# Optimization experiments

Measured on AMD Instinct MI355X. Metric: run time of the kernel, lower is better.

## Reference

```python
import jax, jax.numpy as jnp
import numpy as np

N = 100000
E = 3200000
IN_DIM = 128
OUT_DIM = 128
BN_EPS = 1e-5
LEAKY_SLOPE = 0.01


def setup_inputs() -> dict:
    key = jax.random.key(0)
    ks = jax.random.split(key, 6)
    fea = jax.random.normal(ks[0], (N, IN_DIM), dtype=jnp.float32)
    edges = jax.random.randint(ks[1], (2, E), 0, N, dtype=jnp.int64)
    Wlin = jax.random.normal(ks[2], (IN_DIM, IN_DIM), dtype=jnp.float32) * (1.0 / np.sqrt(IN_DIM))
    blin = jax.random.normal(ks[3], (IN_DIM,), dtype=jnp.float32) * 0.01
    gamma = jnp.ones((IN_DIM,), dtype=jnp.float32)
    beta = jnp.zeros((IN_DIM,), dtype=jnp.float32)
    Wg = jax.random.normal(ks[4], (OUT_DIM, IN_DIM), dtype=jnp.float32) * (1.0 / np.sqrt(IN_DIM))
    bg = jnp.zeros((OUT_DIM,), dtype=jnp.float32)
    return {"fea": fea, "edges": edges, "Wlin": Wlin, "blin": blin,
            "gamma": gamma, "beta": beta, "Wg": Wg, "bg": bg}


def reference(fea, edges, Wlin, blin, gamma, beta, Wg, bg):
    n = fea.shape[0]
    # Linear (in_dim -> in_dim)
    x = fea @ Wlin.T + blin
    # BatchNorm1d, training-mode batch statistics over the node dimension
    mean = jnp.mean(x, axis=0)
    var = jnp.var(x, axis=0)
    x = gamma * (x - mean) * jax.lax.rsqrt(var + BN_EPS) + beta
    # Dropout(p=0.0) is identity; LeakyReLU
    x = jnp.where(x >= 0, x, LEAKY_SLOPE * x)
    # GCNConv: h = x W^T, then D^-1/2 (A+I) D^-1/2 aggregation + bias
    h = x @ Wg.T  # [N, out_dim]
    self_idx = jnp.arange(n, dtype=edges.dtype)
    src = jnp.concatenate([edges[0], self_idx])
    dst = jnp.concatenate([edges[1], self_idx])
    deg = jax.ops.segment_sum(jnp.ones_like(dst, dtype=h.dtype), dst, num_segments=n)
    dinv = jnp.where(deg > 0, jax.lax.rsqrt(deg), 0.0)
    norm = dinv[src] * dinv[dst]  # [E+N]
    msgs = norm[:, None] * h[src]  # [E+N, out_dim]
    out = jax.ops.segment_sum(msgs, dst, num_segments=n) + bg
    # LogSoftmax over feature dim
    return jax.nn.log_softmax(out, axis=1)
```

## Files before the change

kernel.cpp:

```cpp
#include <hip/hip_runtime.h>
#include <math.h>

#define LEAKY 0.01f
#define BN_EPS 1e-5f
#define NBLK 480
#define EBUF 10240

typedef unsigned int uint;
typedef float f32x2 __attribute__((ext_vector_type(2)));
typedef float f32x4 __attribute__((ext_vector_type(4)));
typedef short bf16x8 __attribute__((ext_vector_type(8)));

__device__ __forceinline__ float bflo(uint v) { return __uint_as_float(v << 16); }
__device__ __forceinline__ float bfhi(uint v) { return __uint_as_float(v & 0xffff0000u); }
__device__ __forceinline__ uint packbf(float a, float b) {
    uint ua = __float_as_uint(a), ub = __float_as_uint(b);
    ua += 0x7fffu + ((ua >> 16) & 1u);
    ub += 0x7fffu + ((ub >> 16) & 1u);
    return (ua >> 16) | (ub & 0xffff0000u);
}

__device__ __forceinline__ int detect_i64(const int* __restrict__ raw) {
    int t = threadIdx.x & 63;
    unsigned long long b = __ballot(raw[2 * t + 1] != 0);
    return b == 0ull;
}

__device__ __forceinline__ void build_bbase_wide(const int* __restrict__ btot,
                                                 int NBUK, int* bb, int* sd)
{
    const int t = threadIdx.x;
    int a0 = 0, a1 = 0, s = 0;
    if (t < 256) {
        a0 = (2 * t     < NBUK) ? btot[2 * t]     : 0;
        a1 = (2 * t + 1 < NBUK) ? btot[2 * t + 1] : 0;
        s = a0 + a1;
        sd[t] = s;
    }
    __syncthreads();
    for (int o = 1; o < 256; o <<= 1) {
        int u = (t >= o && t < 256) ? sd[t - o] : 0;
        __syncthreads();
        if (t < 256) sd[t] += u;
        __syncthreads();
    }
    if (t < 256) {
        int ex = sd[t] - s;
        bb[2 * t]     = ex;
        bb[2 * t + 1] = ex + a0;
    }
    __syncthreads();
}

__global__ __launch_bounds__(256) void k_prep(const float* __restrict__ Wlin,
                                              const float* __restrict__ Wg,
                                              uint* __restrict__ Wlinb,
                                              uint* __restrict__ Wgb,
                                              float* __restrict__ sumsr)
{
    const int idx = blockIdx.x * 256 + threadIdx.x;
    if (blockIdx.x < 32) sumsr[blockIdx.x * 256 + threadIdx.x] = 0.f;
    if (idx < 8192) {
        Wlinb[idx] = packbf(Wlin[2 * idx], Wlin[2 * idx + 1]);
    } else {
        int j = idx - 8192;
        Wgb[j] = packbf(Wg[2 * j], Wg[2 * j + 1]);
    }
}

__global__ __launch_bounds__(256) void k_front(const float* __restrict__ fea,
                                               const uint* __restrict__ Wb,
                                               const float* __restrict__ bias,
                                               uint* __restrict__ xb,
                                               float* __restrict__ sumsr,
                                               const void* __restrict__ edges, int E,
                                               int* __restrict__ histm,
                                               int NBUK, int N, int G_lin)
{
    __shared__ uint smem[4352];
    const int tid = threadIdx.x;

    if ((int)blockIdx.x >= G_lin) {
        const int bid = blockIdx.x - G_lin;
        int* hh = (int*)smem;
        for (int b = tid; b < 512; b += 256) hh[b] = 0;
        const int isI64 = detect_i64((const int*)edges);
        __syncthreads();
        const long long* e64 = (const long long*)edges;
        const int*       e32 = (const int*)edges;
        const int chunk = (E + NBLK - 1) / NBLK;
        const int lo = bid * chunk;
        const int hi = min(lo + chunk, E);
        for (int e = lo + tid; e < hi; e += 256) {
            int dst = isI64 ? (int)e64[(size_t)E + e] : e32[(size_t)E + e];
            atomicAdd(&hh[dst >> 8], 1);
        }
        __syncthreads();
        for (int b = tid; b < NBUK; b += 256)
            histm[(size_t)b * NBLK + bid] = hh[b];
        return;
    }

    const int r0   = blockIdx.x * 64;
    const int lane = tid & 63;
    const int w    = tid >> 6;
    const int fr   = lane & 15;
    const int fk   = lane >> 4;
    const int gr_a = r0 + w * 16 + fr;

    bf16x8 a[4];
    #pragma unroll
    for (int kk = 0; kk < 4; ++kk) {
        float4 q0 = make_float4(0.f, 0.f, 0.f, 0.f), q1 = q0;
        if (gr_a < N) {
            const float* fp = &fea[(size_t)gr_a * 128 + 32 * kk + 8 * fk];
            q0 = *reinterpret_cast<const float4*>(fp);
            q1 = *reinterpret_cast<const float4*>(fp + 4);
        }
        uint4 uu = make_uint4(packbf(q0.x, q0.y), packbf(q0.z, q0.w),
                              packbf(q1.x, q1.y), packbf(q1.z, q1.w));
        a[kk] = *reinterpret_cast<bf16x8*>(&uu);
    }

    f32x4 acc[8] = {};
    #pragma unroll
    for (int jt = 0; jt < 8; ++jt) {
        #pragma unroll
        for (int kk = 0; kk < 4; ++kk) {
            bf16x8 b = *reinterpret_cast<const bf16x8*>(
                &Wb[(size_t)(jt * 16 + fr) * 64 + kk * 16 + fk * 4]);
            acc[jt] = __builtin_amdgcn_mfma_f32_16x16x32_bf16(a[kk], b, acc[jt], 0, 0, 0);
        }
    }

    float* sred = (float*)smem;
    float* qred = sred + 2048;
    #pragma unroll
    for (int jt = 0; jt < 8; ++jt) {
        float bj = bias[jt * 16 + fr];
        float sl = 0.f, ql = 0.f;
        #pragma unroll
        for (int r = 0; r < 4; ++r) {
            int gr = r0 + w * 16 + fk * 4 + r;
            float val = acc[jt][r] + bj;
            val = (gr < N) ? val : 0.f;
            acc[jt][r] = val;
            sl += val; ql += val * val;
        }
        sred[(w * 4 + fk) * 128 + jt * 16 + fr] = sl;
        qred[(w * 4 + fk) * 128 + jt * 16 + fr] = ql;
    }
    __syncthreads();
    if (tid < 128) {
        float S = 0.f, Q = 0.f;
        #pragma unroll
        for (int g = 0; g < 16; ++g) {
            S += sred[g * 128 + tid];
            Q += qred[g * 128 + tid];
        }
        float* dstp = sumsr + (blockIdx.x & 31) * 256;
        atomicAdd(&dstp[tid], S);
        atomicAdd(&dstp[128 + tid], Q);
    }
    __syncthreads();

    #pragma unroll
    for (int jt = 0; jt < 8; ++jt) {
        #pragma unroll
        for (int r = 0; r < 4; ++r) {
            float val = acc[jt][r];
            float pv  = __shfl_xor(val, 1);
            if ((lane & 1) == 0)
                smem[(w * 16 + fk * 4 + r) * 68 + jt * 8 + (fr >> 1)] = packbf(val, pv);
        }
    }
    __syncthreads();
    #pragma unroll
    for (int it = 0; it < 4; ++it) {
        int idx4 = it * 256 + tid;
        int row  = idx4 >> 4;
        int c4   = idx4 & 15;
        if (r0 + row < N) {
            uint4 v = *reinterpret_cast<const uint4*>(&smem[row * 68 + c4 * 4]);
            *reinterpret_cast<uint4*>(&xb[(size_t)(r0 + row) * 64 + c4 * 4]) = v;
        }
    }
}

__global__ __launch_bounds__(512) void k_bscan(int* __restrict__ histm,
                                               int* __restrict__ btot)
{
    __shared__ int sd[512];
    const int bkt = blockIdx.x;
    const int t = threadIdx.x;
    int v = (t < NBLK) ? histm[(size_t)bkt * NBLK + t] : 0;
    sd[t] = v;
    __syncthreads();
    for (int o = 1; o < 512; o <<= 1) {
        int u = (t >= o) ? sd[t - o] : 0;
        __syncthreads();
        sd[t] += u;
        __syncthreads();
    }
    if (t < NBLK) histm[(size_t)bkt * NBLK + t] = sd[t] - v;
    if (t == 511) btot[bkt] = sd[511];
}

__global__ __launch_bounds__(512) void k_binscatter(const void* __restrict__ edges, int E,
                                                    const int* __restrict__ histm,
                                                    const int* __restrict__ btot,
                                                    uint* __restrict__ bins,
                                                    const float* __restrict__ sumsr,
                                                    const float* __restrict__ gamma,
                                                    const float* __restrict__ beta,
                                                    float invN,
                                                    float* __restrict__ affg,
                                                    int NBUK)
{
    __shared__ int cur[512];
    __shared__ int bb[512];
    __shared__ int sd[256];
    const int isI64 = detect_i64((const int*)edges);

    if (blockIdx.x == 0 && threadIdx.x < 128) {
        const int tid = threadIdx.x;
        float S = 0.f, Q = 0.f;
        #pragma unroll
        for (int rep = 0; rep < 32; ++rep) {
            S += sumsr[rep * 256 + tid];
            Q += sumsr[rep * 256 + 128 + tid];
        }
        float mean = S * invN;
        float var  = Q * invN - mean * mean;
        float coef = gamma[tid] * rsqrtf(var + BN_EPS);
        affg[tid]       = coef;
        affg[128 + tid] = beta[tid] - coef * mean;
    }

    build_bbase_wide(btot, NBUK, bb, sd);
    for (int b = threadIdx.x; b < NBUK; b += 512)
        cur[b] = bb[b] + histm[(size_t)b * NBLK + blockIdx.x];
    __syncthreads();

    const long long* e64 = (const long long*)edges;
    const int*       e32 = (const int*)edges;
    const int chunk = (E + NBLK - 1) / NBLK;
    const int lo = blockIdx.x * chunk;
    const int hi = min(lo + chunk, E);
    for (int e = lo + threadIdx.x; e < hi; e += 512) {
        int src, dst;
        if (isI64) { src = (int)e64[e]; dst = (int)e64[(size_t)E + e]; }
        else       { src = e32[e];      dst = e32[(size_t)E + e]; }
        int pos = atomicAdd(&cur[dst >> 8], 1);
        bins[pos] = (uint)src | ((uint)(dst & 255) << 24);
    }
}

__global__ __launch_bounds__(1024) void k_csrdeg(const uint* __restrict__ bins,
                                                 const int* __restrict__ btot,
                                                 int* __restrict__ pcnt,
                                                 float* __restrict__ dinv,
                                                 int* __restrict__ offs,
                                                 uint* __restrict__ csr,
                                                 int N, int NBUK)
{
    __shared__ uint ebuf[EBUF];
    __shared__ int bb[512];
    __shared__ int sd[256];
    __shared__ int c[256];
    const int bkt = blockIdx.x;
    const int t = threadIdx.x;
    build_bbase_wide(btot, NBUK, bb, sd);
    const int lo    = bb[bkt];
    const int total = btot[bkt];
    if (t < 256) c[t] = 0;
    __syncthreads();

    const bool fits = (total <= EBUF);
    for (int i = t; i < total; i += 1024) {
        uint e = bins[lo + i];
        if (fits) ebuf[i] = e;
        atomicAdd(&c[e >> 24], 1);
    }
    __syncthreads();

    const int node = (bkt << 8) + t;
    int deg = 0, pdeg = 0;
    if (t < 256) {
        deg  = c[t];
        pdeg = (deg + 15) & ~15;
        if (node < N) {
            pcnt[node] = pdeg;
            dinv[node] = rsqrtf((float)(deg + 1));
        }
        sd[t] = pdeg;
    }
    __syncthreads();
    for (int o = 1; o < 256; o <<= 1) {
        int u = (t >= o && t < 256) ? sd[t - o] : 0;
        __syncthreads();
        if (t < 256) sd[t] += u;
        __syncthreads();
    }
    if (t < 256) {
        const int myoff = lo + (bkt << 12) + sd[t] - pdeg;
        if (node < N) offs[node] = myoff;
        c[t] = myoff;
    }
    __syncthreads();
    for (int i = t; i < total; i += 1024) {
        uint e = fits ? ebuf[i] : bins[lo + i];
        int pos = atomicAdd(&c[e >> 24], 1);
        csr[pos] = e & 0x00ffffffu;
    }
    if (t < 256) {
        const int myoff = lo + (bkt << 12) + sd[t] - pdeg;
        for (int k2 = deg; k2 < pdeg; ++k2)
            csr[myoff + k2] = (uint)N;
    }
}

__global__ __launch_bounds__(256) void k_h(const uint* __restrict__ xb,
                                           const uint* __restrict__ Wb,
                                           const float* __restrict__ affg,
                                           const float* __restrict__ dinv,
                                           uint* __restrict__ hb, int N)
{
    __shared__ uint xls[2304];
    __shared__ float aff[256];
    const int tid  = threadIdx.x;
    const int r0   = blockIdx.x * 64;
    const int lane = tid & 63;
    const int w    = tid >> 6;
    const int fr   = lane & 15;
    const int fk   = lane >> 4;

    aff[tid] = affg[tid & 255];
    __syncthreads();

    const int gr_a = r0 + w * 16 + fr;
    bf16x8 a[4];
    #pragma unroll
    for (int kk = 0; kk < 4; ++kk) {
        uint4 xv = make_uint4(0u, 0u, 0u, 0u);
        if (gr_a < N)
            xv = *reinterpret_cast<const uint4*>(&xb[(size_t)gr_a * 64 + kk * 16 + fk * 4]);
        const int fb = 2 * (kk * 16 + fk * 4);
        uint uv[4] = {xv.x, xv.y, xv.z, xv.w};
        uint ou[4];
        #pragma unroll
        for (int t2 = 0; t2 < 4; ++t2) {
            float y0 = fmaf(aff[fb + 2 * t2],     bflo(uv[t2]), aff[128 + fb + 2 * t2]);
            float y1 = fmaf(aff[fb + 2 * t2 + 1], bfhi(uv[t2]), aff[128 + fb + 2 * t2 + 1]);
            y0 = (y0 >= 0.f) ? y0 : LEAKY * y0;
            y1 = (y1 >= 0.f) ? y1 : LEAKY * y1;
            ou[t2] = packbf(y0, y1);
        }
        uint4 uu = make_uint4(ou[0], ou[1], ou[2], ou[3]);
        a[kk] = *reinterpret_cast<bf16x8*>(&uu);
    }

    f32x4 acc[8] = {};
    #pragma unroll
    for (int jt = 0; jt < 8; ++jt) {
        #pragma unroll
        for (int kk = 0; kk < 4; ++kk) {
            bf16x8 b = *reinterpret_cast<const bf16x8*>(
                &Wb[(size_t)(jt * 16 + fr) * 64 + kk * 16 + fk * 4]);
            acc[jt] = __builtin_amdgcn_mfma_f32_16x16x32_bf16(a[kk], b, acc[jt], 0, 0, 0);
        }
    }

    float dv[4];
    #pragma unroll
    for (int r = 0; r < 4; ++r) {
        int gr = r0 + w * 16 + fk * 4 + r;
        dv[r] = (gr < N) ? dinv[gr] : 0.f;
    }

    #pragma unroll
    for (int jt = 0; jt < 8; ++jt) {
        #pragma unroll
        for (int r = 0; r < 4; ++r) {
            float val = acc[jt][r] * dv[r];
            float p1  = __shfl_xor(val, 1);
            uint lo16 = (uint)__builtin_amdgcn_cvt_pk_fp8_f32(val, p1, 0, false) & 0xffffu;
            uint hi16 = __shfl_xor(lo16, 2);
            if ((fr & 3) == 0)
                xls[(w * 16 + fk * 4 + r) * 36 + jt * 4 + (fr >> 2)] = lo16 | (hi16 << 16);
        }
    }
    __syncthreads();
    #pragma unroll
    for (int it = 0; it < 2; ++it) {
        int idx4 = it * 256 + tid;
        int row  = idx4 >> 3;
        int c4   = idx4 & 7;
        if (r0 + row <= N) {
            uint4 v = *reinterpret_cast<const uint4*>(&xls[row * 36 + c4 * 4]);
            *reinterpret_cast<uint4*>(&hb[(size_t)(r0 + row) * 32 + c4 * 4]) = v;
        }
    }
}

__global__ __launch_bounds__(256) void k_agg(const uint* __restrict__ hb,
                                             const uint* __restrict__ csr,
                                             const int* __restrict__ offs,
                                             const int* __restrict__ pcnt,
                                             const float* __restrict__ dinv,
                                             const float* __restrict__ bg,
                                             float* __restrict__ out, int N)
{
    const int wid  = (blockIdx.x * blockDim.x + threadIdx.x) >> 6;
    const int lane = threadIdx.x & 63;
    if (wid >= N) return;
    const int i = wid;
    const int p = lane & 15;
    const int q = lane >> 4;
    const uint2* hbp = reinterpret_cast<const uint2*>(hb) + p;

    f32x2 acc[4] = {};
    const int start = offs[i];
    const int m     = pcnt[i];

    for (int base = 0; base < m; base += 64) {
        const int nb = min(64, m - base);
        uint sx = (uint)N;
        if (lane < nb)
            sx = __builtin_nontemporal_load(&csr[start + base + lane]);
        for (int j = 0; j < nb; j += 16) {
            int s0 = __shfl((int)sx, j + q);
            int s1 = __shfl((int)sx, j + 4 + q);
            int s2 = __shfl((int)sx, j + 8 + q);
            int s3 = __shfl((int)sx, j + 12 + q);
            const uint2 v0 = hbp[(uint)s0 * 16];
            const uint2 v1 = hbp[(uint)s1 * 16];
            const uint2 v2 = hbp[(uint)s2 * 16];
            const uint2 v3 = hbp[(uint)s3 * 16];
            acc[0] += __builtin_amdgcn_cvt_pk_f32_fp8((int)v0.x, false);
            acc[1] += __builtin_amdgcn_cvt_pk_f32_fp8((int)v0.x, true);
            acc[2] += __builtin_amdgcn_cvt_pk_f32_fp8((int)v0.y, false);
            acc[3] += __builtin_amdgcn_cvt_pk_f32_fp8((int)v0.y, true);
            acc[0] += __builtin_amdgcn_cvt_pk_f32_fp8((int)v1.x, false);
            acc[1] += __builtin_amdgcn_cvt_pk_f32_fp8((int)v1.x, true);
            acc[2] += __builtin_amdgcn_cvt_pk_f32_fp8((int)v1.y, false);
            acc[3] += __builtin_amdgcn_cvt_pk_f32_fp8((int)v1.y, true);
            acc[0] += __builtin_amdgcn_cvt_pk_f32_fp8((int)v2.x, false);
            acc[1] += __builtin_amdgcn_cvt_pk_f32_fp8((int)v2.x, true);
            acc[2] += __builtin_amdgcn_cvt_pk_f32_fp8((int)v2.y, false);
            acc[3] += __builtin_amdgcn_cvt_pk_f32_fp8((int)v2.y, true);
            acc[0] += __builtin_amdgcn_cvt_pk_f32_fp8((int)v3.x, false);
            acc[1] += __builtin_amdgcn_cvt_pk_f32_fp8((int)v3.x, true);
            acc[2] += __builtin_amdgcn_cvt_pk_f32_fp8((int)v3.y, false);
            acc[3] += __builtin_amdgcn_cvt_pk_f32_fp8((int)v3.y, true);
        }
    }

    #pragma unroll
    for (int r = 0; r < 4; ++r) {
        acc[r].x += __shfl_xor(acc[r].x, 16);
        acc[r].y += __shfl_xor(acc[r].y, 16);
        acc[r].x += __shfl_xor(acc[r].x, 32);
        acc[r].y += __shfl_xor(acc[r].y, 32);
    }

    const uint2 sv = hbp[(uint)i * 16];
    acc[0] += __builtin_amdgcn_cvt_pk_f32_fp8((int)sv.x, false);
    acc[1] += __builtin_amdgcn_cvt_pk_f32_fp8((int)sv.x, true);
    acc[2] += __builtin_amdgcn_cvt_pk_f32_fp8((int)sv.y, false);
    acc[3] += __builtin_amdgcn_cvt_pk_f32_fp8((int)sv.y, true);

    const float d0 = dinv[i];
    float4 b0 = *reinterpret_cast<const float4*>(&bg[p * 8]);
    float4 b1 = *reinterpret_cast<const float4*>(&bg[p * 8 + 4]);
    float v0 = fmaf(d0, acc[0].x, b0.x);
    float v1 = fmaf(d0, acc[0].y, b0.y);
    float v2 = fmaf(d0, acc[1].x, b0.z);
    float v3 = fmaf(d0, acc[1].y, b0.w);
    float v4 = fmaf(d0, acc[2].x, b1.x);
    float v5 = fmaf(d0, acc[2].y, b1.y);
    float v6 = fmaf(d0, acc[3].x, b1.z);
    float v7 = fmaf(d0, acc[3].y, b1.w);

    float mx = fmaxf(fmaxf(fmaxf(v0, v1), fmaxf(v2, v3)),
                     fmaxf(fmaxf(v4, v5), fmaxf(v6, v7)));
    #pragma unroll
    for (int o = 8; o > 0; o >>= 1) mx = fmaxf(mx, __shfl_xor(mx, o));
    float sum = __expf(v0 - mx) + __expf(v1 - mx) + __expf(v2 - mx) + __expf(v3 - mx)
              + __expf(v4 - mx) + __expf(v5 - mx) + __expf(v6 - mx) + __expf(v7 - mx);
    #pragma unroll
    for (int o = 8; o > 0; o >>= 1) sum += __shfl_xor(sum, o);
    float ls = mx + __logf(sum);

    if (q == 0) {
        f32x4 o0 = {v0 - ls, v1 - ls, v2 - ls, v3 - ls};
        f32x4 o1 = {v4 - ls, v5 - ls, v6 - ls, v7 - ls};
        __builtin_nontemporal_store(o0, reinterpret_cast<f32x4*>(&out[(size_t)i * 128 + p * 8]));
        __builtin_nontemporal_store(o1, reinterpret_cast<f32x4*>(&out[(size_t)i * 128 + p * 8 + 4]));
    }
}

extern "C" void kernel_launch(void* const* d_in, const int* in_sizes, int n_in,
                              void* d_out, int out_size, void* d_ws, size_t ws_size,
                              hipStream_t stream)
{
    (void)n_in; (void)out_size; (void)ws_size;
    const float* fea   = (const float*)d_in[0];
    const void*  edges = d_in[1];
    const float* Wlin  = (const float*)d_in[2];
    const float* blin  = (const float*)d_in[3];
    const float* gamma = (const float*)d_in[4];
    const float* beta  = (const float*)d_in[5];
    const float* Wg    = (const float*)d_in[6];
    const float* bg    = (const float*)d_in[7];
    float* out = (float*)d_out;

    const int N    = in_sizes[0] / 128;
    const int E    = in_sizes[1] / 2;
    const int NBUK = (N + 255) >> 8;
    const int GLIN = (N + 63) / 64;
    const float invN = 1.0f / (float)N;

    char* p = (char*)d_ws;
    uint*  xb   = (uint*)p;    p += (size_t)N * 64 * 4;
    uint*  bins = (uint*)p;    p += (size_t)E * 4;
    uint*  hb   = (uint*)p;    p += ((size_t)N + 1) * 32 * 4;
    uint*  csr  = (uint*)p;    p += ((size_t)E + ((size_t)NBUK << 12)) * 4;
    int*   histm = (int*)p;    p += (size_t)NBUK * NBLK * 4;
    float* sumsr = (float*)p;  p += 32 * 256 * 4;
    int*   pcnt = (int*)p;     p += (size_t)N * 4;
    int*   offs = (int*)p;     p += (size_t)N * 4;
    float* dinv = (float*)p;   p += (size_t)N * 4;
    int*   btot = (int*)p;     p += 512 * 4;
    float* affg = (float*)p;   p += 256 * 4;
    uint*  Wlinb = (uint*)p;   p += 8192 * 4;
    uint*  Wgb   = (uint*)p;   p += 8192 * 4;

    k_prep<<<64, 256, 0, stream>>>(Wlin, Wg, Wlinb, Wgb, sumsr);

    k_front<<<GLIN + NBLK, 256, 0, stream>>>(fea, Wlinb, blin, xb, sumsr,
                                             edges, E, histm, NBUK, N, GLIN);

    k_bscan<<<NBUK, 512, 0, stream>>>(histm, btot);
    k_binscatter<<<NBLK, 512, 0, stream>>>(edges, E, histm, btot, bins,
                                           sumsr, gamma, beta, invN, affg, NBUK);
    k_csrdeg<<<NBUK, 1024, 0, stream>>>(bins, btot, pcnt, dinv, offs, csr, N, NBUK);

    k_h<<<(N + 64) / 64, 256, 0, stream>>>(xb, Wgb, affg, dinv, hb, N);

    k_agg<<<(N + 3) / 4, 256, 0, stream>>>(hb, csr, offs, pcnt, dinv, bg, out, N);
}
```

Measured before the change: 209.0 us.

## Sort nodes by degree class within buckets for aggregation load balance

k_csrdeg now counting-sorts each bucket's 256 nodes by padded-degree class, highest first, and writes a node permutation. k_agg walks that permutation, so waves in the same block handle nodes of similar degree, which is meant to reduce wave divergence and tail imbalance. The aggregation loop also raises wave priority with s_setprio, and the front kernel reads features with nontemporal loads. The cost is an extra indirection load per wave, extra shared atomics in csrdeg, and scattered output rows.

```diff
diff --git a/kernel.cpp b/kernel.cpp
--- a/kernel.cpp
+++ b/kernel.cpp
@@ -111,11 +111,12 @@
     bf16x8 a[4];
     #pragma unroll
     for (int kk = 0; kk < 4; ++kk) {
-        float4 q0 = make_float4(0.f, 0.f, 0.f, 0.f), q1 = q0;
+        f32x4 q0 = {0.f, 0.f, 0.f, 0.f}, q1 = {0.f, 0.f, 0.f, 0.f};
         if (gr_a < N) {
-            const float* fp = &fea[(size_t)gr_a * 128 + 32 * kk + 8 * fk];
-            q0 = *reinterpret_cast<const float4*>(fp);
-            q1 = *reinterpret_cast<const float4*>(fp + 4);
+            const f32x4* fp = reinterpret_cast<const f32x4*>(
+                &fea[(size_t)gr_a * 128 + 32 * kk + 8 * fk]);
+            q0 = __builtin_nontemporal_load(fp);
+            q1 = __builtin_nontemporal_load(fp + 1);
         }
         uint4 uu = make_uint4(packbf(q0.x, q0.y), packbf(q0.z, q0.w),
                               packbf(q1.x, q1.y), packbf(q1.z, q1.w));
@@ -262,18 +263,21 @@
                                                  float* __restrict__ dinv,
                                                  int* __restrict__ offs,
                                                  uint* __restrict__ csr,
+                                                 uint* __restrict__ nodeord,
                                                  int N, int NBUK)
 {
     __shared__ uint ebuf[EBUF];
     __shared__ int bb[512];
     __shared__ int sd[256];
     __shared__ int c[256];
+    __shared__ int clso[32];
     const int bkt = blockIdx.x;
     const int t = threadIdx.x;
     build_bbase_wide(btot, NBUK, bb, sd);
     const int lo    = bb[bkt];
     const int total = btot[bkt];
     if (t < 256) c[t] = 0;
+    if (t >= 256 && t < 288) clso[t - 256] = 0;
     __syncthreads();
 
     const bool fits = (total <= EBUF);
@@ -285,15 +289,28 @@
     __syncthreads();
 
     const int node = (bkt << 8) + t;
-    int deg = 0, pdeg = 0;
+    int deg = 0, pdeg = 0, cls = 0;
     if (t < 256) {
         deg  = c[t];
         pdeg = (deg + 15) & ~15;
+        cls  = min(pdeg >> 4, 31);
         if (node < N) {
             pcnt[node] = pdeg;
             dinv[node] = rsqrtf((float)(deg + 1));
         }
+        atomicAdd(&clso[cls], 1);
         sd[t] = pdeg;
+    }
+    __syncthreads();
+    if (t == 0) {
+        int run = 0;
+        #pragma unroll
+        for (int cc = 31; cc >= 0; --cc) { int v = clso[cc]; clso[cc] = run; run += v; }
+    }
+    __syncthreads();
+    if (t < 256) {
+        int rank = atomicAdd(&clso[cls], 1);
+        nodeord[(bkt << 8) + rank] = (node < N) ? (uint)node : 0xFFFFFFFFu;
     }
     __syncthreads();
     for (int o = 1; o < 256; o <<= 1) {
@@ -409,12 +426,15 @@
                                              const int* __restrict__ pcnt,
                                              const float* __restrict__ dinv,
                                              const float* __restrict__ bg,
-                                             float* __restrict__ out, int N)
-{
-    const int wid  = (blockIdx.x * blockDim.x + threadIdx.x) >> 6;
+                                             const uint* __restrict__ nodeord,
+                                             float* __restrict__ out, int NSLOT, int N)
+{
+    const int slot = (blockIdx.x * blockDim.x + threadIdx.x) >> 6;
     const int lane = threadIdx.x & 63;
-    if (wid >= N) return;
-    const int i = wid;
+    if (slot >= NSLOT) return;
+    const uint ni = nodeord[slot];
+    if (ni >= (uint)N) return;
+    const int i = (int)ni;
     const int p = lane & 15;
     const int q = lane >> 4;
     const uint2* hbp = reinterpret_cast<const uint2*>(hb) + p;
@@ -423,6 +443,7 @@
     const int start = offs[i];
     const int m     = pcnt[i];
 
+    __builtin_amdgcn_s_setprio(1);
     for (int base = 0; base < m; base += 64) {
         const int nb = min(64, m - base);
         uint sx = (uint)N;
@@ -455,6 +476,7 @@
             acc[3] += __builtin_amdgcn_cvt_pk_f32_fp8((int)v3.y, true);
         }
     }
+    __builtin_amdgcn_s_setprio(0);
 
     #pragma unroll
     for (int r = 0; r < 4; ++r) {
@@ -519,6 +541,7 @@
     const int E    = in_sizes[1] / 2;
     const int NBUK = (N + 255) >> 8;
     const int GLIN = (N + 63) / 64;
+    const int NSLOT = NBUK << 8;
     const float invN = 1.0f / (float)N;
 
     char* p = (char*)d_ws;
@@ -533,6 +556,7 @@
     float* dinv = (float*)p;   p += (size_t)N * 4;
     int*   btot = (int*)p;     p += 512 * 4;
     float* affg = (float*)p;   p += 256 * 4;
+    uint*  nodeord = (uint*)p; p += (size_t)NSLOT * 4;
     uint*  Wlinb = (uint*)p;   p += 8192 * 4;
     uint*  Wgb   = (uint*)p;   p += 8192 * 4;
 
@@ -544,9 +568,11 @@
     k_bscan<<<NBUK, 512, 0, stream>>>(histm, btot);
     k_binscatter<<<NBLK, 512, 0, stream>>>(edges, E, histm, btot, bins,
                                            sumsr, gamma, beta, invN, affg, NBUK);
-    k_csrdeg<<<NBUK, 1024, 0, stream>>>(bins, btot, pcnt, dinv, offs, csr, N, NBUK);
+    k_csrdeg<<<NBUK, 1024, 0, stream>>>(bins, btot, pcnt, dinv, offs, csr,
+                                        nodeord, N, NBUK);
 
     k_h<<<(N + 64) / 64, 256, 0, stream>>>(xb, Wgb, affg, dinv, hb, N);
 
-    k_agg<<<(N + 3) / 4, 256, 0, stream>>>(hb, csr, offs, pcnt, dinv, bg, out, N);
-}
+    k_agg<<<(NSLOT + 3) / 4, 256, 0, stream>>>(hb, csr, offs, pcnt, dinv, bg,
+                                               nodeord, out, NSLOT, N);
+}
```

After: 218.5 us. +4.5%, slower.
